# Kernel tuning notes

Hardware: AMD Instinct MI355X
Metric: run time of the kernel (lower is better)

The kernel has to match this reference:

```python
import jax, jax.numpy as jnp
import numpy as np

ALPHA = 0.2        # LeakyReLU negative slope (self.alpha)
NEG = -9e15        # mask value used by the torch module


def gru_cell(x, h, W_ih, W_hh, b_ih, b_hh):
    """torch.nn.GRUCell math. x, h: [N, F]; W_*: [3F, F]; b_*: [3F]. Gate order r,z,n."""
    gi = x @ W_ih.T + b_ih
    gh = h @ W_hh.T + b_hh
    ir, iz, i_n = jnp.split(gi, 3, axis=-1)
    hr, hz, h_n = jnp.split(gh, 3, axis=-1)
    r = jax.nn.sigmoid(ir + hr)
    z = jax.nn.sigmoid(iz + hz)
    n = jnp.tanh(i_n + r * h_n)
    return (1.0 - z) * n + z * h


def setup_inputs() -> dict:
    key = jax.random.key(0)
    N, F = 8192, 256
    ks = jax.random.split(key, 8)
    inputs = jax.random.normal(ks[0], (N, F), jnp.float32)
    # GRUCell parameters
    W_ih = jax.random.normal(ks[1], (3 * F, F), jnp.float32) / np.sqrt(F)
    W_hh = jax.random.normal(ks[2], (3 * F, F), jnp.float32) / np.sqrt(F)
    b_ih = jax.random.normal(ks[3], (3 * F,), jnp.float32) * 0.01
    b_hh = jax.random.normal(ks[4], (3 * F,), jnp.float32) * 0.01
    # GAT attention vector a: [2F, 1]
    a = jax.random.normal(ks[5], (2 * F, 1), jnp.float32) / np.sqrt(2.0 * F)
    # per-node neighbor pair (encodes weight_dict's 1-/2-neighbor cases)
    nbr = jax.random.randint(ks[6], (N, 2), 0, N)
    # dense adjacency, values in {0,1}
    adj = jax.random.randint(ks[7], (N, N), 0, 2).astype(jnp.int32)
    return dict(inputs=inputs, W_ih=W_ih, W_hh=W_hh, b_ih=b_ih, b_hh=b_hh,
                a=a, nbr=nbr, adj=adj)


def reference(inputs, W_ih, W_hh, b_ih, b_hh, a, nbr, adj):
    F_dim = inputs.shape[1]
    # per-node GRU aggregation: hidden = neighbor1 feature, input = neighbor2 feature
    h = inputs[nbr[:, 0]]                      # [N, F]
    x = inputs[nbr[:, 1]]                      # [N, F]
    outs = gru_cell(x, h, W_ih, W_hh, b_ih, b_hh)  # [N, F]
    # GAT scores: e[i,j] = leakyrelu([outs_i || outs_j] . a) = leakyrelu(f1_i + f2_j)
    # (decomposed -- avoids materializing the [N*N, 2F] concat of the original)
    a1 = a[:F_dim, 0]                          # [F]
    a2 = a[F_dim:, 0]                          # [F]
    e = jax.nn.leaky_relu((outs @ a1)[:, None] + (outs @ a2)[None, :], ALPHA)  # [N, N]
    e = jnp.where(adj > 0, e, NEG)
    return jax.nn.softmax(e, axis=1)
```

## Files before the change

kernel.cpp:

```cpp
#include <hip/hip_runtime.h>
#include <hip/hip_bf16.h>

#define NN 8192
#define FF 256
#define NEGV -9000000000000000.0f

typedef __bf16 bf16x8 __attribute__((ext_vector_type(8)));
typedef float f32x4 __attribute__((ext_vector_type(4)));
typedef int i32x4 __attribute__((ext_vector_type(4)));

__device__ __forceinline__ void load_lds16(const void* g, void* l) {
  auto gp = (const __attribute__((address_space(1))) void*)(uintptr_t)g;
  auto lp = (__attribute__((address_space(3))) void*)(uint32_t)(uintptr_t)l;
  __builtin_amdgcn_global_load_lds(gp, lp, 16, 0, 0);
}

__global__ __launch_bounds__(256) void k_convert(const float* __restrict__ inputs,
                                                 const float* __restrict__ Wih,
                                                 const float* __restrict__ Whh,
                                                 __hip_bfloat16* __restrict__ ibf,
                                                 __hip_bfloat16* __restrict__ Wc) {
  const int gid = blockIdx.x * 256 + threadIdx.x;
  const size_t NI = (size_t)NN * FF;
  const size_t base = (size_t)gid * 8;
  const float* src;
  __hip_bfloat16* dst;
  if (base < NI) { src = inputs + base; dst = ibf + base; }
  else {
    const size_t wo = base - NI;
    dst = Wc + wo;
    src = (wo < 196608) ? (Wih + wo) : (Whh + (wo - 196608));
  }
  const float4 v0 = *(const float4*)src;
  const float4 v1 = *(const float4*)(src + 4);
  union { __hip_bfloat16 h[8]; uint4 u; } t;
  t.h[0] = __float2bfloat16(v0.x); t.h[1] = __float2bfloat16(v0.y);
  t.h[2] = __float2bfloat16(v0.z); t.h[3] = __float2bfloat16(v0.w);
  t.h[4] = __float2bfloat16(v1.x); t.h[5] = __float2bfloat16(v1.y);
  t.h[6] = __float2bfloat16(v1.z); t.h[7] = __float2bfloat16(v1.w);
  *(uint4*)dst = t.u;
}

__global__ __launch_bounds__(256) void k_gru(const __hip_bfloat16* __restrict__ ibf,
                                             const __hip_bfloat16* __restrict__ Wc,
                                             const float* __restrict__ inputs,
                                             const int* __restrict__ nbr,
                                             const float* __restrict__ b_ih,
                                             const float* __restrict__ b_hh,
                                             const float* __restrict__ a,
                                             float* __restrict__ p1a,
                                             float* __restrict__ p2a) {
  __shared__ __align__(16) __hip_bfloat16 Ax[32 * 256];
  __shared__ __align__(16) __hip_bfloat16 Ah[32 * 256];
  __shared__ int hrow_s[32];
  __shared__ float r1[4][32], r2[4][32];
  const int rb = blockIdx.x * 32;
  const int fb = blockIdx.y;
  const int tid = threadIdx.x;
  const int w = tid >> 6, l = tid & 63;
  const int fl = l & 15, q = l >> 4;

  if (tid < 32) hrow_s[tid] = nbr[2 * (rb + tid)];

  {
    const int rlb = w * 8;
#pragma unroll
    for (int j = 0; j < 4; ++j) {
      const int r = rlb + j * 2 + (l >> 5);
      const int cs = l & 31;
      const int gc = cs ^ (r & 7);
      const int xr = nbr[2 * (rb + r) + 1];
      const int hr_ = nbr[2 * (rb + r)];
      load_lds16((const char*)(ibf + (size_t)xr * FF) + gc * 16,
                 (char*)Ax + (rlb + j * 2) * 512);
      load_lds16((const char*)(ibf + (size_t)hr_ * FF) + gc * 16,
                 (char*)Ah + (rlb + j * 2) * 512);
    }
  }
  __syncthreads();

  float p1[8] = {0.f, 0.f, 0.f, 0.f, 0.f, 0.f, 0.f, 0.f};
  float p2[8] = {0.f, 0.f, 0.f, 0.f, 0.f, 0.f, 0.f, 0.f};

  const int f = fb * 64 + w * 16 + fl;
  const float bir = b_ih[f], biz = b_ih[256 + f], bin_ = b_ih[512 + f];
  const float bhr = b_hh[f], bhz = b_hh[256 + f], bhn = b_hh[512 + f];
  const float a1f = a[f], a2f = a[256 + f];

  f32x4 acc[6][2];
#pragma unroll
  for (int g = 0; g < 6; ++g) { acc[g][0] = (f32x4){0,0,0,0}; acc[g][1] = (f32x4){0,0,0,0}; }

  bf16x8 af[2][8];
#pragma unroll
  for (int m = 0; m < 2; ++m)
#pragma unroll
    for (int ks = 0; ks < 8; ++ks) {
      const int row = m * 16 + fl;
      const int c = ks * 4 + q;
      af[m][ks] = *(const bf16x8*)((const char*)Ax + row * 512 + (c ^ (row & 7)) * 16);
    }
#pragma unroll
  for (int g = 0; g < 3; ++g) {
    const __hip_bfloat16* bp = Wc + (size_t)(g * 256 + f) * FF + q * 8;
#pragma unroll
    for (int ks = 0; ks < 8; ++ks) {
      const bf16x8 bf = *(const bf16x8*)(bp + ks * 32);
      acc[g][0] = __builtin_amdgcn_mfma_f32_16x16x32_bf16(af[0][ks], bf, acc[g][0], 0, 0, 0);
      acc[g][1] = __builtin_amdgcn_mfma_f32_16x16x32_bf16(af[1][ks], bf, acc[g][1], 0, 0, 0);
    }
  }
#pragma unroll
  for (int m = 0; m < 2; ++m)
#pragma unroll
    for (int ks = 0; ks < 8; ++ks) {
      const int row = m * 16 + fl;
      const int c = ks * 4 + q;
      af[m][ks] = *(const bf16x8*)((const char*)Ah + row * 512 + (c ^ (row & 7)) * 16);
    }
#pragma unroll
  for (int g = 0; g < 3; ++g) {
    const __hip_bfloat16* bp = Wc + (size_t)(768 + g * 256 + f) * FF + q * 8;
#pragma unroll
    for (int ks = 0; ks < 8; ++ks) {
      const bf16x8 bf = *(const bf16x8*)(bp + ks * 32);
      acc[3 + g][0] = __builtin_amdgcn_mfma_f32_16x16x32_bf16(af[0][ks], bf, acc[3 + g][0], 0, 0, 0);
      acc[3 + g][1] = __builtin_amdgcn_mfma_f32_16x16x32_bf16(af[1][ks], bf, acc[3 + g][1], 0, 0, 0);
    }
  }

#pragma unroll
  for (int m = 0; m < 2; ++m)
#pragma unroll
    for (int j = 0; j < 4; ++j) {
      const int row = m * 16 + q * 4 + j;
      const float ir = acc[0][m][j] + bir;
      const float iz = acc[1][m][j] + biz;
      const float in_ = acc[2][m][j] + bin_;
      const float hrv = acc[3][m][j] + bhr;
      const float hzv = acc[4][m][j] + bhz;
      const float hnv = acc[5][m][j] + bhn;
      const float r_ = 1.f / (1.f + __expf(-(ir + hrv)));
      const float z_ = 1.f / (1.f + __expf(-(iz + hzv)));
      const float n_ = tanhf(in_ + r_ * hnv);
      const float hval = inputs[(size_t)hrow_s[row] * FF + f];
      const float o = (1.f - z_) * n_ + z_ * hval;
      p1[m * 4 + j] += o * a1f;
      p2[m * 4 + j] += o * a2f;
    }

#pragma unroll
  for (int i = 0; i < 8; ++i) {
#pragma unroll
    for (int off = 1; off < 16; off <<= 1) {
      p1[i] += __shfl_xor(p1[i], off);
      p2[i] += __shfl_xor(p2[i], off);
    }
  }
  if (fl == 0) {
#pragma unroll
    for (int m = 0; m < 2; ++m)
#pragma unroll
      for (int j = 0; j < 4; ++j) {
        const int row = m * 16 + q * 4 + j;
        r1[w][row] = p1[m * 4 + j];
        r2[w][row] = p2[m * 4 + j];
      }
  }
  __syncthreads();
  if (tid < 32) {
    p1a[fb * NN + rb + tid] = r1[0][tid] + r1[1][tid] + r1[2][tid] + r1[3][tid];
  } else if (tid < 64) {
    const int t2 = tid - 32;
    p2a[fb * NN + rb + t2] = r2[0][t2] + r2[1][t2] + r2[2][t2] + r2[3][t2];
  }
}

__global__ __launch_bounds__(256) void k_reduce(const float* __restrict__ p1a,
                                                const float* __restrict__ p2a,
                                                float* __restrict__ s1,
                                                float* __restrict__ s2) {
  const int i = blockIdx.x * 256 + threadIdx.x;
  s1[i] = p1a[i] + p1a[NN + i] + p1a[2 * NN + i] + p1a[3 * NN + i];
  s2[i] = p2a[i] + p2a[NN + i] + p2a[2 * NN + i] + p2a[3 * NN + i];
}

__global__ __launch_bounds__(256) void k_softmax(const int* __restrict__ adj,
                                                 const float* __restrict__ s1,
                                                 const float* __restrict__ s2,
                                                 float* __restrict__ out) {
  __shared__ float red[4];
  const int row = blockIdx.x;
  const int t = threadIdx.x;
  const i32x4* adjv = (const i32x4*)(adj + (size_t)row * NN);
  i32x4 a4[8];
#pragma unroll
  for (int k = 0; k < 8; ++k) a4[k] = __builtin_nontemporal_load(adjv + k * 256 + t);
  f32x4 sv[8];
#pragma unroll
  for (int k = 0; k < 8; ++k) sv[k] = *(const f32x4*)(s2 + (k * 256 + t) * 4);
  const float s1v = s1[row];

  float e[32];
  float tsum = 0.f;
#pragma unroll
  for (int k = 0; k < 8; ++k) {
#pragma unroll
    for (int c = 0; c < 4; ++c) {
      float x = s1v + sv[k][c];
      x = (x > 0.f) ? x : 0.2f * x;
      x = (a4[k][c] > 0) ? x : NEGV;
      x = __expf(x);
      e[4 * k + c] = x;
      tsum += x;
    }
  }
#pragma unroll
  for (int off = 32; off; off >>= 1) tsum += __shfl_xor(tsum, off);
  if ((t & 63) == 0) red[t >> 6] = tsum;
  __syncthreads();
  const float inv = 1.f / (red[0] + red[1] + red[2] + red[3]);
  float* orow = out + (size_t)row * NN;
#pragma unroll
  for (int k = 0; k < 8; ++k) {
    const int v = k * 256 + t;
    f32x4 o;
#pragma unroll
    for (int c = 0; c < 4; ++c) o[c] = e[4 * k + c] * inv;
    __builtin_nontemporal_store(o, (f32x4*)(orow + v * 4));
  }
}

extern "C" void kernel_launch(void* const* d_in, const int* in_sizes, int n_in,
                              void* d_out, int out_size, void* d_ws, size_t ws_size,
                              hipStream_t stream) {
  const float* inputs = (const float*)d_in[0];
  const float* W_ih   = (const float*)d_in[1];
  const float* W_hh   = (const float*)d_in[2];
  const float* b_ih   = (const float*)d_in[3];
  const float* b_hh   = (const float*)d_in[4];
  const float* a      = (const float*)d_in[5];
  const int*   nbr    = (const int*)d_in[6];
  const int*   adj    = (const int*)d_in[7];
  float* out = (float*)d_out;

  __hip_bfloat16* ibf = (__hip_bfloat16*)((char*)d_out + (64u << 20));
  __hip_bfloat16* Wc  = (__hip_bfloat16*)((char*)d_out + (80u << 20));
  float* p1a = (float*)((char*)d_out + (96u << 20));
  float* p2a = p1a + 4 * NN;
  float* s1 = (float*)d_ws;
  float* s2 = s1 + NN;

  k_convert<<<1216, 256, 0, stream>>>(inputs, W_ih, W_hh, ibf, Wc);
  k_gru<<<dim3(256, 4), 256, 0, stream>>>(ibf, Wc, inputs, nbr, b_ih, b_hh, a, p1a, p2a);
  k_reduce<<<32, 256, 0, stream>>>(p1a, p2a, s1, s2);
  k_softmax<<<NN, 256, 0, stream>>>(adj, s1, s2, out);
}
```

Baseline: 132.7 us.

## Pre-pack GRU weights in MFMA fragment order and batch four rows per softmax block

The convert kernel now writes the bf16 weights in an order that matches the per-lane MFMA B-fragment layout, so each wave's weight loads in the GRU kernel become contiguous 16-byte-per-lane coalesced reads instead of strided row reads. The softmax kernel processes four rows per block, reusing the s2 vector loaded into registers across rows and cutting the grid from 8192 to 2048 blocks. In exchange, each softmax block runs four passes one after another, with extra syncs and fewer blocks in flight to hide memory latency.

```diff
diff --git a/kernel.cpp b/kernel.cpp
--- a/kernel.cpp
+++ b/kernel.cpp
@@ -21,15 +21,23 @@
                                                  __hip_bfloat16* __restrict__ ibf,
                                                  __hip_bfloat16* __restrict__ Wc) {
   const int gid = blockIdx.x * 256 + threadIdx.x;
-  const size_t NI = (size_t)NN * FF;
-  const size_t base = (size_t)gid * 8;
   const float* src;
   __hip_bfloat16* dst;
-  if (base < NI) { src = inputs + base; dst = ibf + base; }
-  else {
-    const size_t wo = base - NI;
-    dst = Wc + wo;
-    src = (wo < 196608) ? (Wih + wo) : (Whh + (wo - 196608));
+  if (gid < 262144) {
+    src = inputs + (size_t)gid * 8;
+    dst = ibf + (size_t)gid * 8;
+  } else {
+    const int o = gid - 262144;
+    const int l = o & 63;
+    const int ks = (o >> 6) & 7;
+    const int w = (o >> 9) & 3;
+    const int fbb = (o >> 11) & 3;
+    const int g = o >> 13;
+    const int row = g * 256 + fbb * 64 + w * 16 + (l & 15);
+    const int col = (l >> 4) * 8 + ks * 32;
+    src = (row < 768) ? (Wih + (size_t)row * FF + col)
+                      : (Whh + (size_t)(row - 768) * FF + col);
+    dst = Wc + (size_t)o * 8;
   }
   const float4 v0 = *(const float4*)src;
   const float4 v1 = *(const float4*)(src + 4);
@@ -42,7 +50,7 @@
 }
 
 __global__ __launch_bounds__(256) void k_gru(const __hip_bfloat16* __restrict__ ibf,
-                                             const __hip_bfloat16* __restrict__ Wc,
+                                             const __hip_bfloat16* __restrict__ Wpk,
                                              const float* __restrict__ inputs,
                                              const int* __restrict__ nbr,
                                              const float* __restrict__ b_ih,
@@ -102,10 +110,10 @@
     }
 #pragma unroll
   for (int g = 0; g < 3; ++g) {
-    const __hip_bfloat16* bp = Wc + (size_t)(g * 256 + f) * FF + q * 8;
-#pragma unroll
-    for (int ks = 0; ks < 8; ++ks) {
-      const bf16x8 bf = *(const bf16x8*)(bp + ks * 32);
+    const int bbase = ((g * 16 + fb * 4 + w) * 8) * 64 + l;
+#pragma unroll
+    for (int ks = 0; ks < 8; ++ks) {
+      const bf16x8 bf = *(const bf16x8*)(Wpk + (size_t)(bbase + ks * 64) * 8);
       acc[g][0] = __builtin_amdgcn_mfma_f32_16x16x32_bf16(af[0][ks], bf, acc[g][0], 0, 0, 0);
       acc[g][1] = __builtin_amdgcn_mfma_f32_16x16x32_bf16(af[1][ks], bf, acc[g][1], 0, 0, 0);
     }
@@ -120,10 +128,10 @@
     }
 #pragma unroll
   for (int g = 0; g < 3; ++g) {
-    const __hip_bfloat16* bp = Wc + (size_t)(768 + g * 256 + f) * FF + q * 8;
-#pragma unroll
-    for (int ks = 0; ks < 8; ++ks) {
-      const bf16x8 bf = *(const bf16x8*)(bp + ks * 32);
+    const int bbase = (((3 + g) * 16 + fb * 4 + w) * 8) * 64 + l;
+#pragma unroll
+    for (int ks = 0; ks < 8; ++ks) {
+      const bf16x8 bf = *(const bf16x8*)(Wpk + (size_t)(bbase + ks * 64) * 8);
       acc[3 + g][0] = __builtin_amdgcn_mfma_f32_16x16x32_bf16(af[0][ks], bf, acc[3 + g][0], 0, 0, 0);
       acc[3 + g][1] = __builtin_amdgcn_mfma_f32_16x16x32_bf16(af[1][ks], bf, acc[3 + g][1], 0, 0, 0);
     }
@@ -189,45 +197,49 @@
                                                  const float* __restrict__ s1,
                                                  const float* __restrict__ s2,
                                                  float* __restrict__ out) {
-  __shared__ float red[4];
-  const int row = blockIdx.x;
+  __shared__ float red[4][4];
   const int t = threadIdx.x;
-  const i32x4* adjv = (const i32x4*)(adj + (size_t)row * NN);
-  i32x4 a4[8];
-#pragma unroll
-  for (int k = 0; k < 8; ++k) a4[k] = __builtin_nontemporal_load(adjv + k * 256 + t);
   f32x4 sv[8];
 #pragma unroll
   for (int k = 0; k < 8; ++k) sv[k] = *(const f32x4*)(s2 + (k * 256 + t) * 4);
-  const float s1v = s1[row];
-
-  float e[32];
-  float tsum = 0.f;
-#pragma unroll
-  for (int k = 0; k < 8; ++k) {
-#pragma unroll
-    for (int c = 0; c < 4; ++c) {
-      float x = s1v + sv[k][c];
-      x = (x > 0.f) ? x : 0.2f * x;
-      x = (a4[k][c] > 0) ? x : NEGV;
-      x = __expf(x);
-      e[4 * k + c] = x;
-      tsum += x;
-    }
-  }
-#pragma unroll
-  for (int off = 32; off; off >>= 1) tsum += __shfl_xor(tsum, off);
-  if ((t & 63) == 0) red[t >> 6] = tsum;
-  __syncthreads();
-  const float inv = 1.f / (red[0] + red[1] + red[2] + red[3]);
-  float* orow = out + (size_t)row * NN;
-#pragma unroll
-  for (int k = 0; k < 8; ++k) {
-    const int v = k * 256 + t;
-    f32x4 o;
-#pragma unroll
-    for (int c = 0; c < 4; ++c) o[c] = e[4 * k + c] * inv;
-    __builtin_nontemporal_store(o, (f32x4*)(orow + v * 4));
+
+#pragma unroll
+  for (int rr = 0; rr < 4; ++rr) {
+    const int row = blockIdx.x * 4 + rr;
+    const i32x4* adjv = (const i32x4*)(adj + (size_t)row * NN);
+    i32x4 a4[8];
+#pragma unroll
+    for (int k = 0; k < 8; ++k) a4[k] = __builtin_nontemporal_load(adjv + k * 256 + t);
+    const float s1v = s1[row];
+
+    float e[32];
+    float tsum = 0.f;
+#pragma unroll
+    for (int k = 0; k < 8; ++k) {
+#pragma unroll
+      for (int c = 0; c < 4; ++c) {
+        float x = s1v + sv[k][c];
+        x = (x > 0.f) ? x : 0.2f * x;
+        x = (a4[k][c] > 0) ? x : NEGV;
+        x = __expf(x);
+        e[4 * k + c] = x;
+        tsum += x;
+      }
+    }
+#pragma unroll
+    for (int off = 32; off; off >>= 1) tsum += __shfl_xor(tsum, off);
+    if ((t & 63) == 0) red[rr][t >> 6] = tsum;
+    __syncthreads();
+    const float inv = 1.f / (red[rr][0] + red[rr][1] + red[rr][2] + red[rr][3]);
+    float* orow = out + (size_t)row * NN;
+#pragma unroll
+    for (int k = 0; k < 8; ++k) {
+      const int v = k * 256 + t;
+      f32x4 o;
+#pragma unroll
+      for (int c = 0; c < 4; ++c) o[c] = e[4 * k + c] * inv;
+      __builtin_nontemporal_store(o, (f32x4*)(orow + v * 4));
+    }
   }
 }
 
@@ -245,14 +257,14 @@
   float* out = (float*)d_out;
 
   __hip_bfloat16* ibf = (__hip_bfloat16*)((char*)d_out + (64u << 20));
-  __hip_bfloat16* Wc  = (__hip_bfloat16*)((char*)d_out + (80u << 20));
+  __hip_bfloat16* Wpk = (__hip_bfloat16*)((char*)d_out + (80u << 20));
   float* p1a = (float*)((char*)d_out + (96u << 20));
   float* p2a = p1a + 4 * NN;
   float* s1 = (float*)d_ws;
   float* s2 = s1 + NN;
 
-  k_convert<<<1216, 256, 0, stream>>>(inputs, W_ih, W_hh, ibf, Wc);
-  k_gru<<<dim3(256, 4), 256, 0, stream>>>(ibf, Wc, inputs, nbr, b_ih, b_hh, a, p1a, p2a);
+  k_convert<<<1216, 256, 0, stream>>>(inputs, W_ih, W_hh, ibf, Wpk);
+  k_gru<<<dim3(256, 4), 256, 0, stream>>>(ibf, Wpk, inputs, nbr, b_ih, b_hh, a, p1a, p2a);
   k_reduce<<<32, 256, 0, stream>>>(p1a, p2a, s1, s2);
-  k_softmax<<<NN, 256, 0, stream>>>(adj, s1, s2, out);
-}
+  k_softmax<<<2048, 256, 0, stream>>>(adj, s1, s2, out);
+}
```

Result: no change. 134.3 us (+1.2%).
